# Kernel tuning notes

Hardware: AMD Instinct MI355X
Metric: run time of the kernel (lower is better)

## Reference

```python
import jax, jax.numpy as jnp
import numpy as np

N_QUBITS = 8
N_QLAYERS = 4
N_HEADS = 4
DIM = 2 ** N_QUBITS  # 256


def layer_norm(x, g, b, eps=1e-5):
    m = x.mean(-1, keepdims=True)
    v = ((x - m) ** 2).mean(-1, keepdims=True)
    return (x - m) / jnp.sqrt(v + eps) * g + b


def rx_mat(theta):
    # theta: scalar or [B]; returns [...,2,2] complex64
    h = theta * 0.5
    c = jnp.cos(h).astype(jnp.complex64)
    s = (jnp.sin(h) * (-1j)).astype(jnp.complex64)
    return jnp.stack([jnp.stack([c, s], -1), jnp.stack([s, c], -1)], -2)


def rz_mat(theta):
    h = (theta * 0.5).astype(jnp.complex64)
    e0 = jnp.exp(-1j * h)
    e1 = jnp.exp(1j * h)
    z = jnp.zeros_like(e0)
    return jnp.stack([jnp.stack([e0, z], -1), jnp.stack([z, e1], -1)], -2)


def apply_1q(state, U, wire, n):
    # state: [B, 2**n]; U: [2,2] (shared) or [B,2,2] (per-sample)
    B = state.shape[0]
    left = 2 ** wire
    right = 2 ** (n - 1 - wire)
    s = state.reshape(B, left, 2, right)
    if U.ndim == 2:
        s = jnp.einsum('jk,blkr->bljr', U, s)
    else:
        s = jnp.einsum('bjk,blkr->bljr', U, s)
    return s.reshape(B, 2 ** n)


def apply_cnot(state, ctrl, n):
    # CNOT with control=ctrl, target=ctrl+1 (adjacent wires)
    B = state.shape[0]
    left = 2 ** ctrl
    right = 2 ** (n - 2 - ctrl)
    s = state.reshape(B, left, 4, right)
    s = s[:, :, jnp.array([0, 1, 3, 2]), :]  # swap |10> and |11>
    return s.reshape(B, 2 ** n)


def quantum_expvals(angles, weights):
    # angles: [B, n_qubits] data-encoding angles; weights: [n_layers, 2, n_qubits]
    # Batched statevector sim of: RX(a_i)RZ(a_i) encoding, then per layer
    # RX(w[l,0,i]) RZ(w[l,1,i]) and a CNOT chain; returns <Z_i> per wire.
    n = N_QUBITS
    B = angles.shape[0]
    state = jnp.zeros((B, 2 ** n), jnp.complex64).at[:, 0].set(1.0)
    for i in range(n):
        state = apply_1q(state, rx_mat(angles[:, i]), i, n)
        state = apply_1q(state, rz_mat(angles[:, i]), i, n)
    for l in range(N_QLAYERS):
        for i in range(n):
            state = apply_1q(state, rx_mat(weights[l, 0, i]), i, n)
            state = apply_1q(state, rz_mat(weights[l, 1, i]), i, n)
        for i in range(n - 1):
            state = apply_cnot(state, i, n)
    probs = jnp.abs(state) ** 2  # [B, 2**n] float32
    zs = []
    for i in range(n):
        p = probs.reshape(B, 2 ** i, 2, 2 ** (n - 1 - i)).sum(axis=(1, 3))
        zs.append(p[:, 0] - p[:, 1])
    return jnp.stack(zs, -1)  # [B, n_qubits]


def mha(x, in_w, in_b, out_w, out_b):
    B, S, d = x.shape
    hd = d // N_HEADS
    qkv = x @ in_w.T + in_b  # [B,S,3d]
    q, k, v = jnp.split(qkv, 3, axis=-1)
    sp = lambda t: t.reshape(B, S, N_HEADS, hd).transpose(0, 2, 1, 3)
    q, k, v = sp(q), sp(k), sp(v)
    scores = jnp.einsum('bhqd,bhkd->bhqk', q, k) / np.sqrt(hd).astype(np.float32)
    attn = jax.nn.softmax(scores, axis=-1)
    o = jnp.einsum('bhqk,bhkd->bhqd', attn, v).transpose(0, 2, 1, 3).reshape(B, S, d)
    return o @ out_w.T + out_b


def _forward(x, attn_in_w, attn_in_b, attn_out_w, attn_out_b,
             ln1_g, ln1_b, ln2_g, ln2_b, ln3_g, ln3_b,
             qin_w, qin_b, qweights, qout_w, qout_b,
             ffn_w1, ffn_b1, ffn_w2, ffn_b2):
    attn_out = mha(x, attn_in_w, attn_in_b, attn_out_w, attn_out_b)
    x = layer_norm(x + attn_out, ln1_g, ln1_b)
    x_norm = layer_norm(x, ln3_g, ln3_b)
    B, S, d = x.shape
    flat = x_norm.reshape(B * S, d)
    angles = flat @ qin_w.T + qin_b  # [B*S, n_qubits]
    z = quantum_expvals(angles, qweights)
    q_out = (z @ qout_w.T + qout_b).reshape(B, S, d)
    x = x + q_out
    h = jax.nn.gelu(x @ ffn_w1.T + ffn_b1, approximate=False)  # torch GELU exact
    ffn_out = h @ ffn_w2.T + ffn_b2  # dropout is identity in eval
    return layer_norm(x + ffn_out, ln2_g, ln2_b)


def setup_inputs() -> dict:
    key = jax.random.key(0)
    ks = jax.random.split(key, 10)
    B, S, d, nq, nl = 32, 512, 512, N_QUBITS, N_QLAYERS
    rn = lambda k, sh, sc=0.02: jax.random.normal(k, sh, jnp.float32) * sc
    return {
        'x': jax.random.normal(ks[0], (B, S, d), jnp.float32),
        'attn_in_w': rn(ks[1], (3 * d, d)),
        'attn_in_b': jnp.zeros((3 * d,), jnp.float32),
        'attn_out_w': rn(ks[2], (d, d)),
        'attn_out_b': jnp.zeros((d,), jnp.float32),
        'ln1_g': jnp.ones((d,), jnp.float32), 'ln1_b': jnp.zeros((d,), jnp.float32),
        'ln2_g': jnp.ones((d,), jnp.float32), 'ln2_b': jnp.zeros((d,), jnp.float32),
        'ln3_g': jnp.ones((d,), jnp.float32), 'ln3_b': jnp.zeros((d,), jnp.float32),
        'qin_w': rn(ks[3], (nq, d), 0.05),
        'qin_b': jnp.zeros((nq,), jnp.float32),
        'qweights': jax.random.uniform(ks[4], (nl, 2, nq), jnp.float32, 0.0, 2.0 * np.pi),
        'qout_w': rn(ks[5], (d, nq), 0.1),
        'qout_b': jnp.zeros((d,), jnp.float32),
        'ffn_w1': rn(ks[6], (4 * d, d)),
        'ffn_b1': jnp.zeros((4 * d,), jnp.float32),
        'ffn_w2': rn(ks[7], (d, 4 * d)),
        'ffn_b2': jnp.zeros((d,), jnp.float32),
    }


def reference(x, attn_in_w, attn_in_b, attn_out_w, attn_out_b,
              ln1_g, ln1_b, ln2_g, ln2_b, ln3_g, ln3_b,
              qin_w, qin_b, qweights, qout_w, qout_b,
              ffn_w1, ffn_b1, ffn_w2, ffn_b2):
    return _forward(x, attn_in_w, attn_in_b, attn_out_w, attn_out_b,
                    ln1_g, ln1_b, ln2_g, ln2_b, ln3_g, ln3_b,
                    qin_w, qin_b, qweights, qout_w, qout_b,
                    ffn_w1, ffn_b1, ffn_w2, ffn_b2)
```

## Files before the change

### kernel.cpp

```cpp
#include <hip/hip_runtime.h>
#include <math.h>


typedef __bf16 bf16;
typedef bf16 bf16x8 __attribute__((ext_vector_type(8)));
typedef bf16 bf16x4 __attribute__((ext_vector_type(4)));
typedef float f32x4 __attribute__((ext_vector_type(4)));

__device__ __forceinline__ void gld16(const void* g, void* l) {
  __builtin_amdgcn_global_load_lds(
      (__attribute__((address_space(1))) void*)(void*)g,
      (__attribute__((address_space(3))) void*)l, 16, 0, 0);
}

__device__ __forceinline__ float waveAllSum(float v) {
#pragma unroll
  for (int m = 1; m < 64; m <<= 1) v += __shfl_xor(v, m, 64);
  return v;
}

__global__ __launch_bounds__(256) void cvt_all(
    const float* __restrict__ x, const float* __restrict__ w1,
    const float* __restrict__ w2, const float* __restrict__ w3,
    const float* __restrict__ w4, bf16* __restrict__ xb,
    bf16* __restrict__ b1, bf16* __restrict__ b2, bf16* __restrict__ b3,
    bf16* __restrict__ b4) {
  int i = blockIdx.x * 256 + threadIdx.x;
  const float* src;
  bf16* dst;
  int off;
  if (i < 2097152) {
    src = x; dst = xb; off = i;
  } else if (i < 2097152 + 196608) {
    src = w1; dst = b1; off = i - 2097152;
  } else if (i < 2097152 + 196608 + 65536) {
    src = w2; dst = b2; off = i - (2097152 + 196608);
  } else if (i < 2097152 + 196608 + 65536 + 262144) {
    src = w3; dst = b3; off = i - (2097152 + 196608 + 65536);
  } else {
    src = w4; dst = b4; off = i - (2097152 + 196608 + 65536 + 262144);
  }
  float4 v = ((const float4*)src)[off];
  bf16x4 o = {(bf16)v.x, (bf16)v.y, (bf16)v.z, (bf16)v.w};
  ((bf16x4*)dst)[off] = o;
}

__global__ void make_gates(const float* __restrict__ qw,
                           float* __restrict__ gates) {
  int t = threadIdx.x;
  if (t >= 32) return;
  int l = t >> 3, i = t & 7;
  float ax = qw[l * 16 + i] * 0.5f;
  float az = qw[l * 16 + 8 + i] * 0.5f;
  float cx, sx, cz, sz;
  sincosf(ax, &sx, &cx);
  sincosf(az, &sz, &cz);
  float* g = gates + t * 8;
  g[0] = cz * cx;   g[1] = -sz * cx;
  g[2] = -sz * sx;  g[3] = -cz * sx;
  g[4] = sz * sx;   g[5] = -cz * sx;
  g[6] = cz * cx;   g[7] = sz * cx;
}

__global__ __launch_bounds__(256) void make_W(const float* __restrict__ gates,
                                              bf16* __restrict__ Wp) {
  int tid = threadIdx.x, lane = tid & 63;
  int k = blockIdx.x * 4 + (tid >> 6);

  float sr[4], si[4];
#pragma unroll
  for (int l = 0; l < 4; ++l) {
    sr[l] = (lane * 4 + l == k) ? 1.0f : 0.0f;
    si[l] = 0.0f;
  }

  auto gate = [&](int p, float u00r, float u00i, float u01r, float u01i,
                  float u10r, float u10i, float u11r, float u11i) {
    if (p >= 2) {
      int m = 1 << (p - 2);
      int b = (lane >> (p - 2)) & 1;
      float csr = b ? u11r : u00r;
      float csi = b ? u11i : u00i;
      float cor = b ? u10r : u01r;
      float coi = b ? u10i : u01i;
#pragma unroll
      for (int l = 0; l < 4; ++l) {
        float pr = __shfl_xor(sr[l], m, 64);
        float pi = __shfl_xor(si[l], m, 64);
        float nr = fmaf(csr, sr[l],
                        fmaf(-csi, si[l], fmaf(cor, pr, -coi * pi)));
        float ni = fmaf(csr, si[l],
                        fmaf(csi, sr[l], fmaf(cor, pi, coi * pr)));
        sr[l] = nr;
        si[l] = ni;
      }
    } else {
      float nr[4], ni[4];
#pragma unroll
      for (int l = 0; l < 4; ++l) {
        int b = (l >> p) & 1;
        int pl = l ^ (1 << p);
        float csr = b ? u11r : u00r;
        float csi = b ? u11i : u00i;
        float cor = b ? u10r : u01r;
        float coi = b ? u10i : u01i;
        nr[l] = fmaf(csr, sr[l],
                     fmaf(-csi, si[l], fmaf(cor, sr[pl], -coi * si[pl])));
        ni[l] = fmaf(csr, si[l],
                     fmaf(csi, sr[l], fmaf(cor, si[pl], coi * sr[pl])));
      }
#pragma unroll
      for (int l = 0; l < 4; ++l) {
        sr[l] = nr[l];
        si[l] = ni[l];
      }
    }
  };
  auto docnot = [&](int i) {
    int pc = 7 - i, pt = 6 - i;
    if (pt >= 2) {
      int ctrl = (lane >> (pc - 2)) & 1;
      int m = 1 << (pt - 2);
#pragma unroll
      for (int l = 0; l < 4; ++l) {
        float pr = __shfl_xor(sr[l], m, 64);
        float pi = __shfl_xor(si[l], m, 64);
        if (ctrl) {
          sr[l] = pr;
          si[l] = pi;
        }
      }
    } else if (pt == 1) {
      if (lane & 1) {
        float t;
        t = sr[0]; sr[0] = sr[2]; sr[2] = t;
        t = si[0]; si[0] = si[2]; si[2] = t;
        t = sr[1]; sr[1] = sr[3]; sr[3] = t;
        t = si[1]; si[1] = si[3]; si[3] = t;
      }
    } else {
      float t;
      t = sr[2]; sr[2] = sr[3]; sr[3] = t;
      t = si[2]; si[2] = si[3]; si[3] = t;
    }
  };

  for (int l = 0; l < 4; ++l) {
    for (int i = 0; i < 8; ++i) {
      const float* g = gates + (l * 8 + i) * 8;
      gate(7 - i, g[0], g[1], g[2], g[3], g[4], g[5], g[6], g[7]);
    }
    for (int i = 0; i < 7; ++i) docnot(i);
  }

#pragma unroll
  for (int l = 0; l < 4; ++l) {
    int j = lane * 4 + l;
    Wp[j * 512 + k] = (bf16)sr[l];
    Wp[j * 512 + 256 + k] = (bf16)(-si[l]);
    Wp[(j + 256) * 512 + k] = (bf16)si[l];
    Wp[(j + 256) * 512 + 256 + k] = (bf16)sr[l];
  }
}

__global__ __launch_bounds__(256) void make_Q(const float* __restrict__ qout_w,
                                              bf16* __restrict__ Q) {
  int t = blockIdx.x * 256 + threadIdx.x;
  int col = t >> 8, k = t & 255;
  float s = 0.f;
#pragma unroll
  for (int w = 0; w < 8; ++w) {
    float sg = ((k >> (7 - w)) & 1) ? -1.0f : 1.0f;
    s = fmaf(qout_w[col * 8 + w], sg, s);
  }
  Q[col * 256 + k] = (bf16)s;
}

__global__ __launch_bounds__(256) void gemm_mfma(
    const bf16* __restrict__ A, const bf16* __restrict__ W,
    const float* __restrict__ bias, const float* __restrict__ Xadd,
    float* __restrict__ Cf, bf16* __restrict__ Cb, bf16* __restrict__ qk,
    bf16* __restrict__ vT, int M, int N, int K, int mode) {
  __shared__ __align__(16) bf16 As[128 * 32];
  __shared__ __align__(16) bf16 Bs[128 * 32];
  int tid = threadIdx.x;
  int lane = tid & 63, w = tid >> 6;
  int wr = w >> 1, wc = w & 1;
  int quad = lane >> 4, lc = lane & 15;
  long m0 = (long)blockIdx.x * 128;
  long n0 = (long)blockIdx.y * 128;
  int r4 = lane >> 2;
  int koff = (lane & 3) * 8;
  f32x4 acc[4][4] = {};

  for (int k0 = 0; k0 < K; k0 += 32) {
    __syncthreads();
#pragma unroll
    for (int p = 0; p < 2; ++p) {
      int row = p * 64 + w * 16 + r4;
      gld16(A + (m0 + row) * (long)K + k0 + koff, &As[row * 32 + koff]);
      gld16(W + (n0 + row) * (long)K + k0 + koff, &Bs[row * 32 + koff]);
    }
    __syncthreads();
    bf16x8 af[4], bfr[4];
#pragma unroll
    for (int i = 0; i < 4; ++i) {
      af[i] = *(const bf16x8*)&As[(wr * 64 + i * 16 + lc) * 32 + quad * 8];
      bfr[i] = *(const bf16x8*)&Bs[(wc * 64 + i * 16 + lc) * 32 + quad * 8];
    }
#pragma unroll
    for (int i = 0; i < 4; ++i)
#pragma unroll
      for (int j = 0; j < 4; ++j)
        acc[i][j] = __builtin_amdgcn_mfma_f32_16x16x32_bf16(af[i], bfr[j],
                                                            acc[i][j], 0, 0, 0);
  }

#pragma unroll
  for (int i = 0; i < 4; ++i) {
    long grow0 = m0 + wr * 64 + i * 16 + quad * 4;
#pragma unroll
    for (int j = 0; j < 4; ++j) {
      long col = n0 + wc * 64 + j * 16 + lc;
      float bv = (mode == 3) ? 0.f : bias[col];
      float v[4];
#pragma unroll
      for (int r = 0; r < 4; ++r) v[r] = acc[i][j][r] + bv;
      if (mode == 0) {
#pragma unroll
        for (int r = 0; r < 4; ++r) Cf[(grow0 + r) * N + col] = v[r];
      } else if (mode == 1) {
#pragma unroll
        for (int r = 0; r < 4; ++r) {
          float g = 0.5f * v[r] * (1.0f + erff(v[r] * 0.70710678118654752f));
          Cb[(grow0 + r) * N + col] = (bf16)g;
        }
      } else if (mode == 3) {
#pragma unroll
        for (int r = 0; r < 4; ++r) Cb[(grow0 + r) * N + col] = (bf16)v[r];
      } else if (mode == 4) {
#pragma unroll
        for (int r = 0; r < 4; ++r) {
          float val = v[r] + Xadd[(grow0 + r) * N + col];
          Cf[(grow0 + r) * N + col] = val;
          Cb[(grow0 + r) * N + col] = (bf16)val;
        }
      } else {
        if (col < 1024) {
#pragma unroll
          for (int r = 0; r < 4; ++r) qk[(grow0 + r) * 1024 + col] = (bf16)v[r];
        } else {
          int hh = (int)((col - 1024) >> 7);
          int dd = (int)((col - 1024) & 127);
          long bidx = grow0 >> 9;
          int s0 = (int)(grow0 & 511);
          bf16x4 pk = {(bf16)v[0], (bf16)v[1], (bf16)v[2], (bf16)v[3]};
          *(bf16x4*)&vT[(((bidx << 2) + hh) * 128 + dd) * 512 + s0] = pk;
        }
      }
    }
  }
}

__global__ __launch_bounds__(256) void attn_mfma(const bf16* __restrict__ qk,
                                                 const bf16* __restrict__ vT,
                                                 bf16* __restrict__ o) {
  __shared__ __align__(16) bf16 Ks[64 * 128];
  __shared__ __align__(16) bf16 Vt[128 * 64];
  __shared__ __align__(16) bf16 Ps[4][64 * 16];
  int tid = threadIdx.x, lane = tid & 63, w = tid >> 6;
  int quad = lane >> 4, lc = lane & 15;
  int bh = blockIdx.x, b = bh >> 2, h = bh & 3;
  int q0 = blockIdx.y * 64 + w * 16;
  const float scale = 0.08838834764831845f;

  bf16x8 qf[4];
  {
    const bf16* qp =
        qk + ((long)(b * 512 + q0 + lc)) * 1024 + h * 128 + quad * 8;
#pragma unroll
    for (int ks = 0; ks < 4; ++ks) qf[ks] = *(const bf16x8*)(qp + ks * 32);
  }
  f32x4 oacc[8] = {};
  float mrun[4] = {-1e30f, -1e30f, -1e30f, -1e30f};
  float lrun[4] = {0.f, 0.f, 0.f, 0.f};

  const bf16* kbase = qk + (long)b * 512 * 1024 + 512 + h * 128;
  const bf16* vbase = vT + (long)bh * 128 * 512;
  int kr = lane >> 4, ke = (lane & 15) * 8;
  int vr = lane >> 3, ve = (lane & 7) * 8;

  for (int kt = 0; kt < 512; kt += 64) {
    __syncthreads();
#pragma unroll
    for (int c = 0; c < 4; ++c) {
      int row = w * 16 + c * 4 + kr;
      gld16(kbase + (long)(kt + row) * 1024 + ke, &Ks[row * 128 + ke]);
    }
#pragma unroll
    for (int c = 0; c < 4; ++c) {
      int row = w * 32 + c * 8 + vr;
      gld16(vbase + (long)row * 512 + kt + ve, &Vt[row * 64 + ve]);
    }
    __syncthreads();

    float p[4][4];
#pragma unroll
    for (int c = 0; c < 4; ++c) {
      f32x4 a = {};
#pragma unroll
      for (int ks = 0; ks < 4; ++ks) {
        bf16x8 kf = *(const bf16x8*)&Ks[(c * 16 + lc) * 128 + ks * 32 + quad * 8];
        a = __builtin_amdgcn_mfma_f32_16x16x32_bf16(qf[ks], kf, a, 0, 0, 0);
      }
#pragma unroll
      for (int r = 0; r < 4; ++r) p[c][r] = a[r] * scale;
    }

    float alpha[4];
#pragma unroll
    for (int r = 0; r < 4; ++r) {
      float mx = fmaxf(fmaxf(p[0][r], p[1][r]), fmaxf(p[2][r], p[3][r]));
#pragma unroll
      for (int m = 1; m < 16; m <<= 1) mx = fmaxf(mx, __shfl_xor(mx, m, 64));
      float mn = fmaxf(mrun[r], mx);
      alpha[r] = expf(mrun[r] - mn);
      mrun[r] = mn;
      float rs = 0.f;
#pragma unroll
      for (int c = 0; c < 4; ++c) {
        float e = expf(p[c][r] - mn);
        p[c][r] = e;
        rs += e;
      }
#pragma unroll
      for (int m = 1; m < 16; m <<= 1) rs += __shfl_xor(rs, m, 64);
      lrun[r] = lrun[r] * alpha[r] + rs;
    }
#pragma unroll
    for (int n = 0; n < 8; ++n)
#pragma unroll
      for (int r = 0; r < 4; ++r) oacc[n][r] *= alpha[r];

#pragma unroll
    for (int c = 0; c < 4; ++c) {
      bf16x4 pk = {(bf16)p[c][0], (bf16)p[c][1], (bf16)p[c][2], (bf16)p[c][3]};
      *(bf16x4*)&Ps[w][(c * 16 + lc) * 16 + quad * 4] = pk;
    }
    bf16x8 pf[2];
#pragma unroll
    for (int kc = 0; kc < 2; ++kc) {
      bf16x8 t;
#pragma unroll
      for (int jj = 0; jj < 8; ++jj)
        t[jj] = Ps[w][(kc * 32 + quad * 8 + jj) * 16 + lc];
      pf[kc] = t;
    }
#pragma unroll
    for (int n = 0; n < 8; ++n)
#pragma unroll
      for (int kc = 0; kc < 2; ++kc) {
        bf16x8 vf = *(const bf16x8*)&Vt[(n * 16 + lc) * 64 + kc * 32 + quad * 8];
        oacc[n] =
            __builtin_amdgcn_mfma_f32_16x16x32_bf16(pf[kc], vf, oacc[n], 0, 0, 0);
      }
  }

  float linv[4];
#pragma unroll
  for (int r = 0; r < 4; ++r) linv[r] = 1.0f / lrun[r];
  bf16* op = o + ((long)(b * 512 + q0 + quad * 4)) * 512 + h * 128 + lc;
#pragma unroll
  for (int n = 0; n < 8; ++n)
#pragma unroll
    for (int r = 0; r < 4; ++r)
      op[(long)r * 512 + n * 16] = (bf16)(oacc[n][r] * linv[r]);
}

__global__ __launch_bounds__(256) void add_ln_kernel(
    const float* __restrict__ a, const float* __restrict__ b,
    const float* __restrict__ g, const float* __restrict__ be,
    float* __restrict__ out) {
  long row = (blockIdx.x * 256 + threadIdx.x) >> 6;
  int lane = threadIdx.x & 63;
  const float* ar = a + row * 512;
  const float* br = b + row * 512;
  float v[8];
  float s = 0.f;
#pragma unroll
  for (int j = 0; j < 8; ++j) {
    int c = lane + 64 * j;
    v[j] = ar[c] + br[c];
    s += v[j];
  }
  s = waveAllSum(s);
  float mean = s * (1.0f / 512.0f);
  float var = 0.f;
#pragma unroll
  for (int j = 0; j < 8; ++j) {
    float d = v[j] - mean;
    var = fmaf(d, d, var);
  }
  var = waveAllSum(var);
  float rstd = rsqrtf(var * (1.0f / 512.0f) + 1e-5f);
  float* orow = out + row * 512;
#pragma unroll
  for (int j = 0; j < 8; ++j) {
    int c = lane + 64 * j;
    orow[c] = (v[j] - mean) * rstd * g[c] + be[c];
  }
}

__global__ __launch_bounds__(256) void quantum_pre(
    const float* __restrict__ x, const float* __restrict__ attnp,
    const float* __restrict__ g1, const float* __restrict__ b1,
    const float* __restrict__ g3, const float* __restrict__ b3,
    const float* __restrict__ qin_w, const float* __restrict__ qin_b,
    float* __restrict__ x1out, bf16* __restrict__ psi) {
  long row = (blockIdx.x * 256 + threadIdx.x) >> 6;
  int lane = threadIdx.x & 63;
  const float* xr = x + row * 512;
  const float* ar = attnp + row * 512;

  float x1v[8];
  {
    float s = 0.f;
#pragma unroll
    for (int j = 0; j < 8; ++j) {
      int c = lane + 64 * j;
      x1v[j] = xr[c] + ar[c];
      s += x1v[j];
    }
    s = waveAllSum(s);
    float mean = s * (1.0f / 512.0f);
    float var = 0.f;
#pragma unroll
    for (int j = 0; j < 8; ++j) {
      float d = x1v[j] - mean;
      var = fmaf(d, d, var);
    }
    var = waveAllSum(var);
    float rstd = rsqrtf(var * (1.0f / 512.0f) + 1e-5f);
#pragma unroll
    for (int j = 0; j < 8; ++j) {
      int c = lane + 64 * j;
      x1v[j] = (x1v[j] - mean) * rstd * g1[c] + b1[c];
    }
  }
  float* x1row = x1out + row * 512;
#pragma unroll
  for (int j = 0; j < 8; ++j) x1row[lane + 64 * j] = x1v[j];

  float xn[8];
  {
    float s = 0.f;
#pragma unroll
    for (int j = 0; j < 8; ++j) s += x1v[j];
    s = waveAllSum(s);
    float mean = s * (1.0f / 512.0f);
    float var = 0.f;
#pragma unroll
    for (int j = 0; j < 8; ++j) {
      float d = x1v[j] - mean;
      var = fmaf(d, d, var);
    }
    var = waveAllSum(var);
    float rstd = rsqrtf(var * (1.0f / 512.0f) + 1e-5f);
#pragma unroll
    for (int j = 0; j < 8; ++j) {
      int c = lane + 64 * j;
      xn[j] = (x1v[j] - mean) * rstd * g3[c] + b3[c];
    }
  }

  float ang[8];
#pragma unroll
  for (int w = 0; w < 8; ++w) {
    float p = 0.f;
#pragma unroll
    for (int j = 0; j < 8; ++j)
      p = fmaf(xn[j], qin_w[w * 512 + lane + 64 * j], p);
    p = waveAllSum(p);
    ang[w] = p + qin_b[w];
  }

  float v0r[8], v0i[8], v1r[8];
#pragma unroll
  for (int i = 0; i < 8; ++i) {
    float h = ang[i] * 0.5f;
    float c, s;
    sincosf(h, &s, &c);
    v0r[i] = c * c;
    v0i[i] = -c * s;
    v1r[i] = s * s;
  }

  float Pr, Pi;
  {
    int bit0 = (lane >> 5) & 1;
    Pr = bit0 ? v1r[0] : v0r[0];
    Pi = v0i[0];
#pragma unroll
    for (int i = 1; i < 6; ++i) {
      int bit = (lane >> (5 - i)) & 1;
      float br = bit ? v1r[i] : v0r[i];
      float bi = v0i[i];
      float nr = Pr * br - Pi * bi;
      float ni = Pr * bi + Pi * br;
      Pr = nr;
      Pi = ni;
    }
  }

  bf16 rebuf[4], imbuf[4];
#pragma unroll
  for (int l = 0; l < 4; ++l) {
    int b6 = (l >> 1) & 1, b7 = l & 1;
    float br = b6 ? v1r[6] : v0r[6], bi = v0i[6];
    float tr = Pr * br - Pi * bi;
    float ti = Pr * bi + Pi * br;
    float cr = b7 ? v1r[7] : v0r[7], ci = v0i[7];
    float fr = tr * cr - ti * ci;
    float fi = tr * ci + ti * cr;
    rebuf[l] = (bf16)fr;
    imbuf[l] = (bf16)fi;
  }
  bf16* prow = psi + row * 512;
  *(bf16x4*)&prow[lane * 4] = *(bf16x4*)rebuf;
  *(bf16x4*)&prow[256 + lane * 4] = *(bf16x4*)imbuf;
}

__global__ __launch_bounds__(256) void prob_kernel(const bf16* __restrict__ phi,
                                                   bf16* __restrict__ prob) {
  int t4 = blockIdx.x * 256 + threadIdx.x;
  int token = t4 >> 6;
  int k4 = (t4 & 63) * 4;
  const bf16* pr = phi + (long)token * 512;
  bf16x4 re = *(const bf16x4*)&pr[k4];
  bf16x4 im = *(const bf16x4*)&pr[256 + k4];
  bf16 ob[4];
#pragma unroll
  for (int l = 0; l < 4; ++l) {
    float r = (float)re[l], i = (float)im[l];
    ob[l] = (bf16)(r * r + i * i);
  }
  *(bf16x4*)&prob[(long)token * 256 + k4] = *(bf16x4*)ob;
}

extern "C" void kernel_launch(void* const* d_in, const int* in_sizes, int n_in,
                              void* d_out, int out_size, void* d_ws,
                              size_t ws_size, hipStream_t stream) {
  const float* x = (const float*)d_in[0];
  const float* attn_in_w = (const float*)d_in[1];
  const float* attn_in_b = (const float*)d_in[2];
  const float* attn_out_w = (const float*)d_in[3];
  const float* attn_out_b = (const float*)d_in[4];
  const float* ln1_g = (const float*)d_in[5];
  const float* ln1_b = (const float*)d_in[6];
  const float* ln2_g = (const float*)d_in[7];
  const float* ln2_b = (const float*)d_in[8];
  const float* ln3_g = (const float*)d_in[9];
  const float* ln3_b = (const float*)d_in[10];
  const float* qin_w = (const float*)d_in[11];
  const float* qin_b = (const float*)d_in[12];
  const float* qweights = (const float*)d_in[13];
  const float* qout_w = (const float*)d_in[14];
  const float* qout_b = (const float*)d_in[15];
  const float* ffn_w1 = (const float*)d_in[16];
  const float* ffn_b1 = (const float*)d_in[17];
  const float* ffn_w2 = (const float*)d_in[18];
  const float* ffn_b2 = (const float*)d_in[19];

  char* wsB = (char*)d_ws;
  bf16* qkb = (bf16*)(wsB);
  bf16* vtb = (bf16*)(wsB + (32L << 20));
  bf16* ob = (bf16*)(wsB + (48L << 20));
  bf16* hb = (bf16*)(wsB);
  float* slot1 = (float*)(wsB + (64L << 20));
  bf16* phi = (bf16*)(wsB + (64L << 20));
  bf16* probb = (bf16*)(wsB + (80L << 20));
  float* f2out = (float*)(wsB + (64L << 20));
  float* x1 = (float*)(wsB + (96L << 20));
  float* x2 = (float*)(wsB + (128L << 20));
  bf16* x2b = (bf16*)(wsB + (160L << 20));
  bf16* xb = (bf16*)(wsB + (176L << 20));
  bf16* psi = (bf16*)(wsB + (176L << 20));
  bf16* w_in = (bf16*)(wsB + (192L << 20));
  bf16* w_out = (bf16*)(wsB + (194L << 20));
  bf16* w_f1 = (bf16*)(wsB + (195L << 20));
  bf16* w_f2 = (bf16*)(wsB + (197L << 20));
  float* gates = (float*)(wsB + (199L << 20));
  bf16* Wp = (bf16*)(wsB + (200L << 20));
  bf16* Qm = (bf16*)(wsB + (201L << 20));

  const int M = 16384;
  float* outp = (float*)d_out;

  cvt_all<<<11264, 256, 0, stream>>>(x, attn_in_w, attn_out_w, ffn_w1, ffn_w2,
                                     xb, w_in, w_out, w_f1, w_f2);
  make_gates<<<1, 64, 0, stream>>>(qweights, gates);
  make_W<<<64, 256, 0, stream>>>(gates, Wp);
  make_Q<<<512, 256, 0, stream>>>(qout_w, Qm);

  gemm_mfma<<<dim3(M / 128, 12), 256, 0, stream>>>(
      xb, w_in, attn_in_b, nullptr, nullptr, nullptr, qkb, vtb, M, 1536, 512,
      2);
  attn_mfma<<<dim3(128, 8), 256, 0, stream>>>(qkb, vtb, ob);
  gemm_mfma<<<dim3(M / 128, 4), 256, 0, stream>>>(
      ob, w_out, attn_out_b, nullptr, slot1, nullptr, nullptr, nullptr, M, 512,
      512, 0);
  quantum_pre<<<dim3(M / 4), 256, 0, stream>>>(x, slot1, ln1_g, ln1_b, ln3_g,
                                               ln3_b, qin_w, qin_b, x1, psi);
  gemm_mfma<<<dim3(M / 128, 4), 256, 0, stream>>>(
      psi, Wp, nullptr, nullptr, nullptr, phi, nullptr, nullptr, M, 512, 512,
      3);
  prob_kernel<<<4096, 256, 0, stream>>>(phi, probb);
  gemm_mfma<<<dim3(M / 128, 4), 256, 0, stream>>>(
      probb, Qm, qout_b, x1, x2, x2b, nullptr, nullptr, M, 512, 256, 4);
  gemm_mfma<<<dim3(M / 128, 16), 256, 0, stream>>>(
      x2b, w_f1, ffn_b1, nullptr, nullptr, hb, nullptr, nullptr, M, 2048, 512,
      1);
  gemm_mfma<<<dim3(M / 128, 4), 256, 0, stream>>>(
      hb, w_f2, ffn_b2, nullptr, f2out, nullptr, nullptr, nullptr, M, 512,
      2048, 0);
  add_ln_kernel<<<dim3(M / 4), 256, 0, stream>>>(x2, f2out, ln2_g, ln2_b,
                                                 outp);
}
```

Measured before the change: 518.5 us.

## Swizzle LDS layouts, widen GEMM K tile, drop online softmax max tracking

```diff
diff --git a/kernel.cpp b/kernel.cpp
--- a/kernel.cpp
+++ b/kernel.cpp
@@ -181,39 +181,45 @@
     const float* __restrict__ bias, const float* __restrict__ Xadd,
     float* __restrict__ Cf, bf16* __restrict__ Cb, bf16* __restrict__ qk,
     bf16* __restrict__ vT, int M, int N, int K, int mode) {
-  __shared__ __align__(16) bf16 As[128 * 32];
-  __shared__ __align__(16) bf16 Bs[128 * 32];
+  __shared__ __align__(16) bf16 As[128 * 64];
+  __shared__ __align__(16) bf16 Bs[128 * 64];
   int tid = threadIdx.x;
   int lane = tid & 63, w = tid >> 6;
   int wr = w >> 1, wc = w & 1;
   int quad = lane >> 4, lc = lane & 15;
   long m0 = (long)blockIdx.x * 128;
   long n0 = (long)blockIdx.y * 128;
-  int r4 = lane >> 2;
-  int koff = (lane & 3) * 8;
   f32x4 acc[4][4] = {};
 
-  for (int k0 = 0; k0 < K; k0 += 32) {
+  int sl0 = w * 256 + lane;
+
+  for (int k0 = 0; k0 < K; k0 += 64) {
     __syncthreads();
 #pragma unroll
-    for (int p = 0; p < 2; ++p) {
-      int row = p * 64 + w * 16 + r4;
-      gld16(A + (m0 + row) * (long)K + k0 + koff, &As[row * 32 + koff]);
-      gld16(W + (n0 + row) * (long)K + k0 + koff, &Bs[row * 32 + koff]);
+    for (int c = 0; c < 4; ++c) {
+      int slot = sl0 + c * 64;
+      int row = slot >> 3, g = slot & 7;
+      int sc = (g ^ (row & 7)) << 3;
+      gld16(A + (m0 + row) * (long)K + k0 + sc, &As[slot << 3]);
+      gld16(W + (n0 + row) * (long)K + k0 + sc, &Bs[slot << 3]);
     }
     __syncthreads();
-    bf16x8 af[4], bfr[4];
-#pragma unroll
-    for (int i = 0; i < 4; ++i) {
-      af[i] = *(const bf16x8*)&As[(wr * 64 + i * 16 + lc) * 32 + quad * 8];
-      bfr[i] = *(const bf16x8*)&Bs[(wc * 64 + i * 16 + lc) * 32 + quad * 8];
-    }
-#pragma unroll
-    for (int i = 0; i < 4; ++i)
-#pragma unroll
-      for (int j = 0; j < 4; ++j)
-        acc[i][j] = __builtin_amdgcn_mfma_f32_16x16x32_bf16(af[i], bfr[j],
-                                                            acc[i][j], 0, 0, 0);
+#pragma unroll
+    for (int t = 0; t < 2; ++t) {
+      bf16x8 af[4], bfr[4];
+      int pg = ((t * 4 + quad) ^ (lc & 7)) << 3;
+#pragma unroll
+      for (int i = 0; i < 4; ++i) {
+        af[i] = *(const bf16x8*)&As[(wr * 64 + i * 16 + lc) * 64 + pg];
+        bfr[i] = *(const bf16x8*)&Bs[(wc * 64 + i * 16 + lc) * 64 + pg];
+      }
+#pragma unroll
+      for (int i = 0; i < 4; ++i)
+#pragma unroll
+        for (int j = 0; j < 4; ++j)
+          acc[i][j] = __builtin_amdgcn_mfma_f32_16x16x32_bf16(
+              af[i], bfr[j], acc[i][j], 0, 0, 0);
+    }
   }
 
 #pragma unroll
@@ -282,25 +288,27 @@
     for (int ks = 0; ks < 4; ++ks) qf[ks] = *(const bf16x8*)(qp + ks * 32);
   }
   f32x4 oacc[8] = {};
-  float mrun[4] = {-1e30f, -1e30f, -1e30f, -1e30f};
   float lrun[4] = {0.f, 0.f, 0.f, 0.f};
 
   const bf16* kbase = qk + (long)b * 512 * 1024 + 512 + h * 128;
   const bf16* vbase = vT + (long)bh * 128 * 512;
-  int kr = lane >> 4, ke = (lane & 15) * 8;
-  int vr = lane >> 3, ve = (lane & 7) * 8;
+  int sl0 = w * 256 + lane;
 
   for (int kt = 0; kt < 512; kt += 64) {
     __syncthreads();
 #pragma unroll
     for (int c = 0; c < 4; ++c) {
-      int row = w * 16 + c * 4 + kr;
-      gld16(kbase + (long)(kt + row) * 1024 + ke, &Ks[row * 128 + ke]);
-    }
-#pragma unroll
-    for (int c = 0; c < 4; ++c) {
-      int row = w * 32 + c * 8 + vr;
-      gld16(vbase + (long)row * 512 + kt + ve, &Vt[row * 64 + ve]);
+      int slot = sl0 + c * 64;
+      {
+        int row = slot >> 4, g = slot & 15;
+        gld16(kbase + (long)(kt + row) * 1024 + ((g ^ (row & 15)) << 3),
+              &Ks[slot << 3]);
+      }
+      {
+        int row = slot >> 3, g = slot & 7;
+        gld16(vbase + (long)row * 512 + kt + ((g ^ (row & 7)) << 3),
+              &Vt[slot << 3]);
+      }
     }
     __syncthreads();
 
@@ -310,57 +318,50 @@
       f32x4 a = {};
 #pragma unroll
       for (int ks = 0; ks < 4; ++ks) {
-        bf16x8 kf = *(const bf16x8*)&Ks[(c * 16 + lc) * 128 + ks * 32 + quad * 8];
+        bf16x8 kf = *(const bf16x8*)&Ks[(c * 16 + lc) * 128 +
+                                        (((ks * 4 + quad) ^ lc) << 3)];
         a = __builtin_amdgcn_mfma_f32_16x16x32_bf16(qf[ks], kf, a, 0, 0, 0);
       }
 #pragma unroll
       for (int r = 0; r < 4; ++r) p[c][r] = a[r] * scale;
     }
 
-    float alpha[4];
 #pragma unroll
     for (int r = 0; r < 4; ++r) {
-      float mx = fmaxf(fmaxf(p[0][r], p[1][r]), fmaxf(p[2][r], p[3][r]));
-#pragma unroll
-      for (int m = 1; m < 16; m <<= 1) mx = fmaxf(mx, __shfl_xor(mx, m, 64));
-      float mn = fmaxf(mrun[r], mx);
-      alpha[r] = expf(mrun[r] - mn);
-      mrun[r] = mn;
       float rs = 0.f;
 #pragma unroll
       for (int c = 0; c < 4; ++c) {
-        float e = expf(p[c][r] - mn);
+        float e = expf(p[c][r]);
         p[c][r] = e;
         rs += e;
       }
 #pragma unroll
       for (int m = 1; m < 16; m <<= 1) rs += __shfl_xor(rs, m, 64);
-      lrun[r] = lrun[r] * alpha[r] + rs;
-    }
-#pragma unroll
-    for (int n = 0; n < 8; ++n)
-#pragma unroll
-      for (int r = 0; r < 4; ++r) oacc[n][r] *= alpha[r];
+      lrun[r] += rs;
+    }
 
 #pragma unroll
     for (int c = 0; c < 4; ++c) {
       bf16x4 pk = {(bf16)p[c][0], (bf16)p[c][1], (bf16)p[c][2], (bf16)p[c][3]};
-      *(bf16x4*)&Ps[w][(c * 16 + lc) * 16 + quad * 4] = pk;
+      *(bf16x4*)&Ps[w][(c * 16 + lc) * 16 + ((quad ^ (lc & 3)) << 2)] = pk;
     }
     bf16x8 pf[2];
 #pragma unroll
     for (int kc = 0; kc < 2; ++kc) {
       bf16x8 t;
 #pragma unroll
-      for (int jj = 0; jj < 8; ++jj)
-        t[jj] = Ps[w][(kc * 32 + quad * 8 + jj) * 16 + lc];
+      for (int jj = 0; jj < 8; ++jj) {
+        int row = kc * 32 + quad * 8 + jj;
+        t[jj] = Ps[w][row * 16 + (((lc >> 2) ^ (row & 3)) << 2) + (lc & 3)];
+      }
       pf[kc] = t;
     }
 #pragma unroll
     for (int n = 0; n < 8; ++n)
 #pragma unroll
       for (int kc = 0; kc < 2; ++kc) {
-        bf16x8 vf = *(const bf16x8*)&Vt[(n * 16 + lc) * 64 + kc * 32 + quad * 8];
+        bf16x8 vf = *(const bf16x8*)&Vt[(n * 16 + lc) * 64 +
+                                        (((kc * 4 + quad) ^ (lc & 7)) << 3)];
         oacc[n] =
             __builtin_amdgcn_mfma_f32_16x16x32_bf16(pf[kc], vf, oacc[n], 0, 0, 0);
       }
```

New measurement: 463.6 us. 10.6% less time.
